# Performance work log

Measured on AMD Instinct MI355X. Metric: run time of the kernel, lower is better.

Reference implementation:

```python
import jax, jax.numpy as jnp
import numpy as np
import math

B, S, HID = 2, 1024, 2048
H, KV, HD = 32, 8, 64
GROUPS = H // KV
KB_N = 4096
THETA = 10000.0


def _rope_cos_sin(position_ids, head_dim, theta=THETA):
    inv_freq = 1.0 / (theta ** (jnp.arange(0, head_dim, 2, dtype=jnp.float32) / head_dim))
    ang = position_ids.astype(jnp.float32)[..., None] * inv_freq  # [B,S,hd/2]
    cos = jnp.concatenate([jnp.cos(ang), jnp.cos(ang)], -1)[:, None]  # [B,1,S,hd]
    sin = jnp.concatenate([jnp.sin(ang), jnp.sin(ang)], -1)[:, None]
    return cos, sin


def _rotate_half(x):
    h = x.shape[-1] // 2
    return jnp.concatenate([-x[..., h:], x[..., :h]], -1)


def _apply_rope(x, cos, sin):
    return x * cos + _rotate_half(x) * sin


def setup_inputs() -> dict:
    key = jax.random.key(0)
    ks = jax.random.split(key, 10)
    hidden_states = jax.random.normal(ks[0], (B, S, HID), dtype=jnp.float32)
    causal = jnp.where(jnp.tril(jnp.ones((S, S), bool)), 0.0, -1e9).astype(jnp.float32)
    attention_mask = jnp.broadcast_to(causal[None, None], (B, 1, S, S)).copy()
    kb_keys = jax.random.normal(ks[1], (B, KB_N, HD), dtype=jnp.float32)
    kb_values = jax.random.normal(ks[2], (B, KB_N, HD), dtype=jnp.float32)
    position_ids = jnp.broadcast_to(jnp.arange(S, dtype=jnp.int64 if jax.config.read('jax_enable_x64') else jnp.int32)[None], (B, S))
    s = 0.02
    Wq = jax.random.normal(ks[3], (HID, HID), dtype=jnp.float32) * s
    Wq_kb = jax.random.normal(ks[4], (HID, HID), dtype=jnp.float32) * s
    Wk = jax.random.normal(ks[5], (KV * HD, HID), dtype=jnp.float32) * s
    Wv = jax.random.normal(ks[6], (KV * HD, HID), dtype=jnp.float32) * s
    Wo = jax.random.normal(ks[7], (HID, HID), dtype=jnp.float32) * s
    score_shift = jnp.zeros((H, 1), dtype=jnp.float32) - 3.0
    return {"hidden_states": hidden_states, "attention_mask": attention_mask,
            "kb_keys": kb_keys, "kb_values": kb_values, "Wq": Wq, "Wq_kb": Wq_kb,
            "Wk": Wk, "Wv": Wv, "Wo": Wo, "score_shift": score_shift,
            "position_ids": position_ids, "top_k": 128}


def reference(hidden_states, attention_mask, kb_keys, kb_values, Wq, Wq_kb, Wk, Wv, Wo, score_shift, position_ids, top_k):
    bsz, q_len, _ = hidden_states.shape
    scale = 1.0 / math.sqrt(HD)
    q = (hidden_states @ Wq.T).reshape(bsz, q_len, H, HD).transpose(0, 2, 1, 3)
    k = (hidden_states @ Wk.T).reshape(bsz, q_len, KV, HD).transpose(0, 2, 1, 3)
    v = (hidden_states @ Wv.T).reshape(bsz, q_len, KV, HD).transpose(0, 2, 1, 3)
    k = jnp.repeat(k, GROUPS, axis=1)  # repeat_kv
    v = jnp.repeat(v, GROUPS, axis=1)
    cos, sin = _rope_cos_sin(position_ids, HD)
    q = _apply_rope(q, cos, sin)
    k = _apply_rope(k, cos, sin)
    attn = jnp.einsum('bhsd,bhtd->bhst', q, k) * scale
    # KB path (layer_idx=0, kb_layer_frequency=1, sep_query_head, dynamic_sparsify)
    qkb = (hidden_states @ Wq_kb.T).reshape(bsz, q_len, H, HD).transpose(0, 2, 1, 3)
    qkb = _apply_rope(qkb, cos, sin)
    kb_scores = jnp.einsum('bhsd,bnd->bhsn', qkb, kb_keys) * scale  # [B,H,S,N]
    # prune_key_value: top-k over head/seq-summed scores, gather keys/values (no grad)
    top_idx = jax.lax.stop_gradient(jax.lax.top_k(kb_scores.sum((1, 2)), top_k)[1])  # [B,k]
    kb_k_g = jax.lax.stop_gradient(jnp.take_along_axis(kb_keys, top_idx[..., None], axis=1))  # [B,k,hd]
    kb_v_g = jax.lax.stop_gradient(jnp.take_along_axis(kb_values, top_idx[..., None], axis=1))
    kb_w = kb_scores[..., :top_k]  # faithful to original: scores of FIRST top_k columns
    kb_w = kb_w + score_shift.reshape(1, H, 1, 1)
    attn_all = jnp.concatenate([attn, kb_w], -1)
    mask_all = jnp.concatenate([attention_mask, jnp.zeros((bsz, 1, q_len, top_k), attention_mask.dtype)], -1)
    attn_all = attn_all + mask_all
    w = jax.nn.softmax(attn_all.astype(jnp.float32), axis=-1).astype(q.dtype)
    out = jnp.einsum('bhst,bhtd->bhsd', w[..., :q_len], v) \
        + jnp.einsum('bhsk,bkd->bhsd', w[..., q_len:], kb_v_g)
    out = out.transpose(0, 2, 1, 3).reshape(bsz, q_len, HID)
    return out @ Wo.T
```

## Files before the change

kernel.cpp:

```cpp
#include <hip/hip_runtime.h>

constexpr int BB   = 2;
constexpr int SEQ  = 1024;
constexpr int HIDC = 2048;
constexpr int NHEAD = 32;
constexpr int NKVH  = 8;
constexpr int HDIM  = 64;
constexpr int KBN   = 4096;
constexpr int TOPK  = 128;
constexpr int HCH   = 16;

typedef unsigned short ushortt;
typedef __attribute__((ext_vector_type(8))) short short8;
typedef __attribute__((ext_vector_type(4))) float f32x4;

__device__ __forceinline__ ushortt f2b(float f){
  union { float f; unsigned u; } v; v.f = f;
  unsigned r = (v.u + 0x7FFFu + ((v.u >> 16) & 1u)) >> 16;
  return (ushortt)r;
}
__device__ __forceinline__ ushortt f2bfast(float f){
  union { float f; unsigned u; } v; v.f = f;
  return (ushortt)((v.u + 0x8000u) >> 16);
}
__device__ __forceinline__ float b2f(ushortt b){
  union { unsigned u; float f; } v; v.u = ((unsigned)b) << 16;
  return v.f;
}
__device__ __forceinline__ void gload16(const void* g, void* l){
  __builtin_amdgcn_global_load_lds((const __attribute__((address_space(1))) void*)g,
                                   (__attribute__((address_space(3))) void*)l, 16, 0, 0);
}

__global__ __launch_bounds__(256) void cast_all(const float* __restrict__ hs,
    const float* __restrict__ Wq, const float* __restrict__ Wqkb,
    const float* __restrict__ Wk, const float* __restrict__ Wv,
    const float* __restrict__ Wo,
    ushortt* __restrict__ hsb, ushortt* __restrict__ Wcatb, ushortt* __restrict__ Wob)
{
  const size_t NHS = (size_t)BB*SEQ*HIDC;
  const size_t NW  = (size_t)5120*HIDC;
  const size_t NO  = (size_t)HIDC*HIDC;
  const size_t total4 = (NHS + NW + NO) / 4;
  for (size_t i = (size_t)blockIdx.x*256 + threadIdx.x; i < total4; i += (size_t)gridDim.x*256){
    size_t e = i * 4;
    const float* src; ushortt* dst;
    if (e < NHS){ src = hs + e; dst = hsb + e; }
    else if (e < NHS + NW){
      size_t ew = e - NHS; dst = Wcatb + ew;
      if      (ew < (size_t)2048*2048) src = Wq   + ew;
      else if (ew < (size_t)4096*2048) src = Wqkb + (ew - (size_t)2048*2048);
      else if (ew < (size_t)4608*2048) src = Wk   + (ew - (size_t)4096*2048);
      else                             src = Wv   + (ew - (size_t)4608*2048);
    } else { size_t eo = e - NHS - NW; src = Wo + eo; dst = Wob + eo; }
    float4 v = *(const float4*)src;
    dst[0] = f2b(v.x); dst[1] = f2b(v.y); dst[2] = f2b(v.z); dst[3] = f2b(v.w);
  }
}

__global__ void rope_table(const int* __restrict__ pos, float* __restrict__ cosT, float* __restrict__ sinT){
  int idx = blockIdx.x*256 + threadIdx.x;
  if (idx >= BB*SEQ*32) return;
  int i = idx & 31; int bs = idx >> 5;
  int p = pos[bs];
  double invf = exp(-(double)i * (log(10000.0) / 32.0));
  double ang = (double)p * invf;
  cosT[idx] = (float)cos(ang);
  sinT[idx] = (float)sin(ang);
}

template<int OUTF32>
__global__ __launch_bounds__(256) void gemm_bt(const ushortt* __restrict__ A,
                                               const ushortt* __restrict__ Bt,
                                               void* __restrict__ Cv,
                                               int M, int N, int K)
{
  __shared__ ushortt As[128*32];
  __shared__ ushortt Bs[128*32];
  const int tid = threadIdx.x;
  const int wave = tid >> 6, lane = tid & 63;
  const int bn = blockIdx.x, bm = blockIdx.y;
  const int wr = (wave >> 1) * 64, wc = (wave & 1) * 64;
  const int l4 = lane >> 4, lm = lane & 15;
  f32x4 acc[4][4] = {};
  const int srow = wave*16 + (lane >> 2);
  const int scol = (lane & 3) * 8;
  const ushortt* Ag0 = A  + (size_t)(bm*128 + srow)*K + scol;
  const ushortt* Ag1 = Ag0 + (size_t)64*K;
  const ushortt* Bg0 = Bt + (size_t)(bn*128 + srow)*K + scol;
  const ushortt* Bg1 = Bg0 + (size_t)64*K;
  ushortt* la0 = &As[(wave*16)*32];
  ushortt* la1 = &As[(64 + wave*16)*32];
  ushortt* lb0 = &Bs[(wave*16)*32];
  ushortt* lb1 = &Bs[(64 + wave*16)*32];
  const int roff = lm*32 + l4*8;
  for (int k0 = 0; k0 < K; k0 += 32){
    gload16(Ag0 + k0, la0);
    gload16(Ag1 + k0, la1);
    gload16(Bg0 + k0, lb0);
    gload16(Bg1 + k0, lb1);
    __syncthreads();
    short8 af[4], bf_[4];
    #pragma unroll
    for (int mi=0;mi<4;++mi) af[mi]  = *(const short8*)&As[(wr + mi*16)*32 + roff];
    #pragma unroll
    for (int ni=0;ni<4;++ni) bf_[ni] = *(const short8*)&Bs[(wc + ni*16)*32 + roff];
    #pragma unroll
    for (int mi=0;mi<4;++mi)
      #pragma unroll
      for (int ni=0;ni<4;++ni)
        acc[mi][ni] = __builtin_amdgcn_mfma_f32_16x16x32_bf16(af[mi], bf_[ni], acc[mi][ni], 0, 0, 0);
    __syncthreads();
  }
  const int cr = l4*4;
  #pragma unroll
  for (int mi=0;mi<4;++mi)
    #pragma unroll
    for (int ni=0;ni<4;++ni)
      #pragma unroll
      for (int r=0;r<4;++r){
        size_t row = (size_t)bm*128 + wr + mi*16 + cr + r;
        size_t col = (size_t)bn*128 + wc + ni*16 + lm;
        float v = acc[mi][ni][r];
        if (OUTF32) ((float*)Cv)[row*(size_t)N + col] = v;
        else        ((ushortt*)Cv)[row*(size_t)N + col] = f2b(v);
      }
}

__global__ __launch_bounds__(256) void rope_pack(const ushortt* __restrict__ C1,
    const float* __restrict__ cosT, const float* __restrict__ sinT,
    ushortt* __restrict__ qr, ushortt* __restrict__ qkbr,
    ushortt* __restrict__ kr, ushortt* __restrict__ vt)
{
  const int row = blockIdx.x;
  const int b = row >> 10, s = row & 1023;
  const ushortt* cr = C1 + (size_t)row * 5120;
  const float* ct = cosT + (size_t)row * 32;
  const float* st = sinT + (size_t)row * 32;
  for (int j = threadIdx.x; j < 2048; j += 256){
    int h = j >> 6, d = j & 63, i = d & 31;
    float c = ct[i], sn = st[i];
    int jp = (d < 32) ? j + 32 : j - 32;
    float x  = b2f(cr[j]);
    float xp = b2f(cr[jp]);
    float o = (d < 32) ? (x*c - xp*sn) : (x*c + xp*sn);
    qr[((size_t)(b*NHEAD + h)*SEQ + s)*HDIM + d] = f2b(o * 0.125f);
    float y  = b2f(cr[2048 + j]);
    float yp = b2f(cr[2048 + jp]);
    float o2 = (d < 32) ? (y*c - yp*sn) : (y*c + yp*sn);
    qkbr[((size_t)(b*NHEAD + h)*SEQ + s)*HDIM + d] = f2b(o2 * 0.125f);
  }
  for (int j = threadIdx.x; j < 512; j += 256){
    int kvh = j >> 6, d = j & 63, i = d & 31;
    float c = ct[i], sn = st[i];
    int jp = (d < 32) ? j + 32 : j - 32;
    float x  = b2f(cr[4096 + j]);
    float xp = b2f(cr[4096 + jp]);
    float o = (d < 32) ? (x*c - xp*sn) : (x*c + xp*sn);
    kr[((size_t)(b*NKVH + kvh)*SEQ + s)*HDIM + d] = f2b(o);
    vt[((size_t)(b*NKVH + kvh)*HDIM + d)*SEQ + s] = cr[4608 + j];
  }
}

__global__ __launch_bounds__(256) void hcs_kernel(const float* __restrict__ hs,
    const float* __restrict__ cosT, const float* __restrict__ sinT,
    float* __restrict__ HcP, float* __restrict__ HsP)
{
  const int b = blockIdx.z, sc = blockIdx.y;
  const int k = blockIdx.x*256 + threadIdx.x;
  const int sbase = sc * (SEQ / HCH);
  __shared__ float cs[64*32];
  __shared__ float sn[64*32];
  for (int t = threadIdx.x; t < 64*32; t += 256){
    cs[t] = cosT[((size_t)b*SEQ + sbase)*32 + t];
    sn[t] = sinT[((size_t)b*SEQ + sbase)*32 + t];
  }
  __syncthreads();
  float ac[32], as_[32];
  #pragma unroll
  for (int i=0;i<32;++i){ ac[i]=0.f; as_[i]=0.f; }
  const float* hp = hs + ((size_t)b*SEQ + sbase)*HIDC + k;
  for (int s = 0; s < 64; ++s){
    float x = hp[(size_t)s*HIDC];
    #pragma unroll
    for (int q=0;q<8;++q){
      float4 c4 = *(const float4*)&cs[s*32 + q*4];
      float4 s4 = *(const float4*)&sn[s*32 + q*4];
      ac[q*4+0]=fmaf(x,c4.x,ac[q*4+0]); as_[q*4+0]=fmaf(x,s4.x,as_[q*4+0]);
      ac[q*4+1]=fmaf(x,c4.y,ac[q*4+1]); as_[q*4+1]=fmaf(x,s4.y,as_[q*4+1]);
      ac[q*4+2]=fmaf(x,c4.z,ac[q*4+2]); as_[q*4+2]=fmaf(x,s4.z,as_[q*4+2]);
      ac[q*4+3]=fmaf(x,c4.w,ac[q*4+3]); as_[q*4+3]=fmaf(x,s4.w,as_[q*4+3]);
    }
  }
  #pragma unroll
  for (int i=0;i<32;++i){
    HcP[(((size_t)sc*BB + b)*32 + i)*HIDC + k] = ac[i];
    HsP[(((size_t)sc*BB + b)*32 + i)*HIDC + k] = as_[i];
  }
}

__global__ __launch_bounds__(256) void hcs_reduce(const float* __restrict__ HcP,
    const float* __restrict__ HsP, float* __restrict__ Hc, float* __restrict__ Hs)
{
  int idx = blockIdx.x*256 + threadIdx.x;
  if (idx >= BB*32*HIDC) return;
  float a = 0.f, c = 0.f;
  #pragma unroll
  for (int sc = 0; sc < HCH; ++sc){
    a += HcP[(size_t)sc*(BB*32*HIDC) + idx];
    c += HsP[(size_t)sc*(BB*32*HIDC) + idx];
  }
  Hc[idx] = a; Hs[idx] = c;
}

__global__ void wsum_kernel(const float* __restrict__ Wqkb, float* __restrict__ Wsum){
  int idx = blockIdx.x*256 + threadIdx.x;
  if (idx >= 64*HIDC) return;
  int d = idx >> 11, k = idx & 2047;
  float acc = 0.f;
  for (int h2 = 0; h2 < NHEAD; ++h2) acc += Wqkb[(size_t)(h2*64 + d)*HIDC + k];
  Wsum[idx] = acc;
}

__global__ __launch_bounds__(256) void qsum_kernel(const float* __restrict__ Hc,
    const float* __restrict__ Hs, const float* __restrict__ Wsum, float* __restrict__ qsum)
{
  const int b = blockIdx.x >> 6, d = blockIdx.x & 63;
  const int i = d & 31;
  const float* hc = Hc + (size_t)(b*32 + i)*HIDC;
  const float* hn = Hs + (size_t)(b*32 + i)*HIDC;
  const float* w1 = Wsum + (size_t)d*HIDC;
  const float* w2 = Wsum + (size_t)((d < 32) ? d + 32 : d - 32)*HIDC;
  double acc = 0.0;
  for (int k = threadIdx.x; k < HIDC; k += 256){
    double t = (double)hc[k] * (double)w1[k];
    double u = (double)hn[k] * (double)w2[k];
    acc += (d < 32) ? (t - u) : (t + u);
  }
  __shared__ double red[256];
  red[threadIdx.x] = acc; __syncthreads();
  for (int s = 128; s > 0; s >>= 1){
    if (threadIdx.x < s) red[threadIdx.x] += red[threadIdx.x + s];
    __syncthreads();
  }
  if (threadIdx.x == 0) qsum[blockIdx.x] = (float)red[0];
}

__global__ void ssum_kernel(const float* __restrict__ qsum, const float* __restrict__ kbK,
                            float* __restrict__ sout){
  int idx = blockIdx.x*256 + threadIdx.x;
  if (idx >= BB*KBN) return;
  int b = idx >> 12;
  const float* q = qsum + b*64;
  const float* kk = kbK + (size_t)idx*64;
  double acc = 0.0;
  for (int d = 0; d < 64; ++d) acc += (double)q[d] * (double)kk[d];
  sout[idx] = (float)(acc * 0.125);
}

__global__ __launch_bounds__(256) void rank_topk(const float* __restrict__ sout,
                                                 int* __restrict__ sel)
{
  const int b = blockIdx.y, chunk = blockIdx.x;
  __shared__ unsigned long long keys[KBN];
  const int tid = threadIdx.x;
  for (int i = tid; i < KBN; i += 256){
    float v = sout[(size_t)b*KBN + i];
    unsigned u = __float_as_uint(v);
    u = (u & 0x80000000u) ? ~u : (u | 0x80000000u);
    keys[i] = ((unsigned long long)u << 32) | (unsigned)(KBN - 1 - i);
  }
  __syncthreads();
  const int myi = chunk*256 + tid;
  const unsigned long long me = keys[myi];
  int rank = 0;
  for (int j = 0; j < KBN; j += 4){
    unsigned long long k0 = keys[j+0];
    unsigned long long k1 = keys[j+1];
    unsigned long long k2 = keys[j+2];
    unsigned long long k3 = keys[j+3];
    rank += (k0 > me) + (k1 > me) + (k2 > me) + (k3 > me);
  }
  if (rank < TOPK) sel[b*TOPK + rank] = myi;
}

__global__ __launch_bounds__(256) void gather_kb(const int* __restrict__ sel,
    const float* __restrict__ kbK, const float* __restrict__ kbV,
    ushortt* __restrict__ kbkb, ushortt* __restrict__ kbvtg)
{
  const int b = blockIdx.x;
  const int tid = threadIdx.x;
  for (int t = tid; t < TOPK*HDIM; t += 256){
    int j = t >> 6, d = t & 63;
    int idx = sel[b*TOPK + j];
    kbkb[(size_t)(b*TOPK + j)*HDIM + d] = f2b(kbK[((size_t)b*KBN + j)*HDIM + d]);
    kbvtg[((size_t)b*HDIM + d)*TOPK + j] = f2b(kbV[((size_t)b*KBN + idx)*HDIM + d]);
  }
}

__global__ __launch_bounds__(256) void attn_kernel(
    const ushortt* __restrict__ qr, const ushortt* __restrict__ qkbr,
    const ushortt* __restrict__ kr, const ushortt* __restrict__ vt,
    const ushortt* __restrict__ kbkb, const ushortt* __restrict__ kbvtg,
    const float* __restrict__ shf, ushortt* __restrict__ attno)
{
  const int i   = blockIdx.x;
  const int xcd = i & 7;
  const int j   = i >> 3;
  const int chunk = xcd + 8*(j >> 5);
  const int pos   = j & 31;
  const int b  = chunk >> 3;
  const int kv = chunk & 7;
  const int qtg = 7 - (pos >> 2);
  const int h  = kv*4 + (pos & 3);
  const int tid = threadIdx.x;
  const int wave = tid >> 6, lane = tid & 63;
  const int l4 = lane >> 4, lm = lane & 15;
  const int qt = qtg*4 + wave;
  const int s0 = qt * 32;

  __shared__ ushortt Ks[2][64*64];
  __shared__ ushortt Vs[2][64*64];
  __shared__ ushortt P[4][32*72];

  ushortt* Pw = P[wave];
  const ushortt* kbase = kr + (size_t)(b*NKVH + kv)*SEQ*HDIM;
  const ushortt* vbase = vt + (size_t)(b*NKVH + kv)*HDIM*SEQ;

  short8 aq[2][2], aqk[2][2];
  {
    const ushortt* qb  = qr   + ((size_t)(b*NHEAD + h)*SEQ + s0)*HDIM;
    const ushortt* qk2 = qkbr + ((size_t)(b*NHEAD + h)*SEQ + s0)*HDIM;
    #pragma unroll
    for (int mi=0;mi<2;++mi)
      #pragma unroll
      for (int kk=0;kk<2;++kk){
        int offa = (mi*16 + lm)*HDIM + kk*32 + l4*8;
        aq[mi][kk]  = *(const short8*)(qb  + offa);
        aqk[mi][kk] = *(const short8*)(qk2 + offa);
      }
  }
  f32x4 O[2][4] = {};
  float lrow[2][4];
  #pragma unroll
  for (int mi=0;mi<2;++mi)
    #pragma unroll
    for (int r=0;r<4;++r) lrow[mi][r] = 0.f;

  auto stageKV = [&](int t, int bsel){
    const int t0 = t*64;
    #pragma unroll
    for (int r2 = 0; r2 < 2; ++r2){
      int slot = r2*256 + wave*64 + lane;
      int row = slot >> 3, cb = slot & 7;
      int lcb = cb ^ (row & 7);
      ushortt* ldsK = &Ks[bsel][(size_t)(r2*256 + wave*64)*8];
      ushortt* ldsV = &Vs[bsel][(size_t)(r2*256 + wave*64)*8];
      gload16(kbase + (size_t)(t0 + row)*HDIM + lcb*8, ldsK);
      gload16(vbase + (size_t)row*SEQ + t0 + lcb*8, ldsV);
    }
  };

  auto update = [&](f32x4 (&lg)[2][4]){
    #pragma unroll
    for (int mi=0;mi<2;++mi)
      #pragma unroll
      for (int r=0;r<4;++r){
        float ps = 0.f;
        #pragma unroll
        for (int ni=0;ni<4;++ni){
          float p = __expf(lg[mi][ni][r]);
          ushortt pb = f2bfast(p);
          ps += b2f(pb);
          Pw[(mi*16 + l4*4 + r)*72 + ni*16 + lm] = pb;
        }
        lrow[mi][r] += ps;
      }
  };

  auto computeTile = [&](int t, int bsel){
    const int t0 = t*64;
    const ushortt* Kb = Ks[bsel];
    const ushortt* Vb = Vs[bsel];
    f32x4 lg[2][4] = {};
    __builtin_amdgcn_s_setprio(1);
    #pragma unroll
    for (int kk=0;kk<2;++kk)
      #pragma unroll
      for (int ni=0;ni<4;++ni){
        int rr = ni*16 + lm;
        int c  = kk*4 + l4;
        short8 bk = *(const short8*)&Kb[rr*64 + ((c ^ (rr&7))*8)];
        lg[0][ni] = __builtin_amdgcn_mfma_f32_16x16x32_bf16(aq[0][kk], bk, lg[0][ni], 0,0,0);
        lg[1][ni] = __builtin_amdgcn_mfma_f32_16x16x32_bf16(aq[1][kk], bk, lg[1][ni], 0,0,0);
      }
    __builtin_amdgcn_s_setprio(0);
    const bool part = (t0 + 63 > s0);
    if (part){
      #pragma unroll
      for (int mi=0;mi<2;++mi)
        #pragma unroll
        for (int ni=0;ni<4;++ni)
          #pragma unroll
          for (int r=0;r<4;++r){
            int row = s0 + mi*16 + l4*4 + r;
            int col = t0 + ni*16 + lm;
            if (col > row) lg[mi][ni][r] = -1e30f;
          }
    }
    update(lg);
    __builtin_amdgcn_s_setprio(1);
    #pragma unroll
    for (int kk=0;kk<2;++kk){
      short8 pa0 = *(const short8*)&Pw[(lm)*72 + kk*32 + l4*8];
      short8 pa1 = *(const short8*)&Pw[(16 + lm)*72 + kk*32 + l4*8];
      #pragma unroll
      for (int di=0;di<4;++di){
        int rr = di*16 + lm;
        int c  = kk*4 + l4;
        short8 bv = *(const short8*)&Vb[rr*64 + ((c ^ (rr&7))*8)];
        O[0][di] = __builtin_amdgcn_mfma_f32_16x16x32_bf16(pa0, bv, O[0][di], 0,0,0);
        O[1][di] = __builtin_amdgcn_mfma_f32_16x16x32_bf16(pa1, bv, O[1][di], 0,0,0);
      }
    }
    __builtin_amdgcn_s_setprio(0);
  };

  const int nkt   = s0/64 + 1;
  const int NTmax = 2*qtg + 2;

  stageKV(0, 0);
  __syncthreads();
  for (int t = 0; t < NTmax; ++t){
    if (t+1 < NTmax) stageKV(t+1, (t+1)&1);
    if (t < nkt) computeTile(t, t&1);
    __syncthreads();
  }

  {
    const float shift = shf[h];
    const ushortt* kbk = kbkb + (size_t)b*TOPK*HDIM;
    const ushortt* kbv = kbvtg + (size_t)b*HDIM*TOPK;
    #pragma unroll
    for (int jt=0;jt<2;++jt){
      const int j0 = jt*64;
      f32x4 lg[2][4] = {};
      __builtin_amdgcn_s_setprio(1);
      #pragma unroll
      for (int kk=0;kk<2;++kk)
        #pragma unroll
        for (int ni=0;ni<4;++ni){
          short8 bk = *(const short8*)(kbk + (size_t)(j0 + ni*16 + lm)*HDIM + kk*32 + l4*8);
          lg[0][ni] = __builtin_amdgcn_mfma_f32_16x16x32_bf16(aqk[0][kk], bk, lg[0][ni], 0,0,0);
          lg[1][ni] = __builtin_amdgcn_mfma_f32_16x16x32_bf16(aqk[1][kk], bk, lg[1][ni], 0,0,0);
        }
      __builtin_amdgcn_s_setprio(0);
      #pragma unroll
      for (int mi=0;mi<2;++mi)
        #pragma unroll
        for (int ni=0;ni<4;++ni)
          #pragma unroll
          for (int r=0;r<4;++r)
            lg[mi][ni][r] += shift;
      update(lg);
      __builtin_amdgcn_s_setprio(1);
      #pragma unroll
      for (int kk=0;kk<2;++kk){
        short8 pa0 = *(const short8*)&Pw[(lm)*72 + kk*32 + l4*8];
        short8 pa1 = *(const short8*)&Pw[(16 + lm)*72 + kk*32 + l4*8];
        #pragma unroll
        for (int di=0;di<4;++di){
          short8 bv = *(const short8*)(kbv + (size_t)(di*16 + lm)*TOPK + j0 + kk*32 + l4*8);
          O[0][di] = __builtin_amdgcn_mfma_f32_16x16x32_bf16(pa0, bv, O[0][di], 0,0,0);
          O[1][di] = __builtin_amdgcn_mfma_f32_16x16x32_bf16(pa1, bv, O[1][di], 0,0,0);
        }
      }
      __builtin_amdgcn_s_setprio(0);
    }
  }
  #pragma unroll
  for (int mi=0;mi<2;++mi)
    #pragma unroll
    for (int r=0;r<4;++r){
      float ls = lrow[mi][r];
      ls += __shfl_xor(ls, 1);
      ls += __shfl_xor(ls, 2);
      ls += __shfl_xor(ls, 4);
      ls += __shfl_xor(ls, 8);
      lrow[mi][r] = 1.0f / ls;
    }
  #pragma unroll
  for (int mi=0;mi<2;++mi)
    #pragma unroll
    for (int di=0;di<4;++di)
      #pragma unroll
      for (int r=0;r<4;++r){
        float o = O[mi][di][r] * lrow[mi][r];
        attno[(size_t)(b*SEQ + s0 + mi*16 + l4*4 + r)*HIDC + h*HDIM + di*16 + lm] = f2b(o);
      }
}

extern "C" void kernel_launch(void* const* d_in, const int* in_sizes, int n_in,
                              void* d_out, int out_size, void* d_ws, size_t ws_size,
                              hipStream_t stream)
{
  (void)in_sizes; (void)n_in; (void)out_size; (void)ws_size;
  const float* hs   = (const float*)d_in[0];
  const float* kbK  = (const float*)d_in[2];
  const float* kbV  = (const float*)d_in[3];
  const float* Wq   = (const float*)d_in[4];
  const float* Wqkb = (const float*)d_in[5];
  const float* Wk   = (const float*)d_in[6];
  const float* Wv   = (const float*)d_in[7];
  const float* Wo   = (const float*)d_in[8];
  const float* shf  = (const float*)d_in[9];
  const int*   pos  = (const int*)d_in[10];

  char* w = (char*)d_ws;
  size_t off = 0;
  auto alloc = [&](size_t bytes)->void*{
    void* p = w + off; off += (bytes + 255) & ~(size_t)255; return p;
  };
  ushortt* hsb   = (ushortt*)alloc((size_t)2048*2048*2);
  ushortt* Wcatb = (ushortt*)alloc((size_t)5120*2048*2);
  ushortt* Wob   = (ushortt*)alloc((size_t)2048*2048*2);
  ushortt* C1    = (ushortt*)alloc((size_t)2048*5120*2);
  float*   cosT  = (float*)alloc((size_t)BB*SEQ*32*4);
  float*   sinT  = (float*)alloc((size_t)BB*SEQ*32*4);
  ushortt* qr    = (ushortt*)alloc((size_t)BB*NHEAD*SEQ*HDIM*2);
  ushortt* qkbr  = (ushortt*)alloc((size_t)BB*NHEAD*SEQ*HDIM*2);
  ushortt* kr    = (ushortt*)alloc((size_t)BB*NKVH*SEQ*HDIM*2);
  ushortt* vt    = (ushortt*)alloc((size_t)BB*NKVH*SEQ*HDIM*2);
  float*   Hc    = (float*)alloc((size_t)BB*32*HIDC*4);
  float*   Hs    = (float*)alloc((size_t)BB*32*HIDC*4);
  float*   Wsum  = (float*)alloc((size_t)64*HIDC*4);
  float*   qsum  = (float*)alloc((size_t)BB*64*4);
  float*   sbuf  = (float*)alloc((size_t)BB*KBN*4);
  int*     sel   = (int*)alloc((size_t)BB*TOPK*4);
  ushortt* kbkb  = (ushortt*)alloc((size_t)BB*TOPK*HDIM*2);
  ushortt* kbvtg = (ushortt*)alloc((size_t)BB*HDIM*TOPK*2);
  ushortt* attno = (ushortt*)alloc((size_t)2048*2048*2);

  float* HcP = (float*)C1;
  float* HsP = HcP + (size_t)HCH*BB*32*HIDC;

  rope_table<<<dim3(256), dim3(256), 0, stream>>>(pos, cosT, sinT);
  hcs_kernel<<<dim3(8, HCH, BB), dim3(256), 0, stream>>>(hs, cosT, sinT, HcP, HsP);
  hcs_reduce<<<dim3(512), dim3(256), 0, stream>>>(HcP, HsP, Hc, Hs);
  wsum_kernel<<<dim3(512), dim3(256), 0, stream>>>(Wqkb, Wsum);
  qsum_kernel<<<dim3(128), dim3(256), 0, stream>>>(Hc, Hs, Wsum, qsum);
  ssum_kernel<<<dim3(32), dim3(256), 0, stream>>>(qsum, kbK, sbuf);
  rank_topk<<<dim3(KBN/256, BB), dim3(256), 0, stream>>>(sbuf, sel);
  gather_kb<<<dim3(BB), dim3(256), 0, stream>>>(sel, kbK, kbV, kbkb, kbvtg);
  cast_all<<<dim3(2048), dim3(256), 0, stream>>>(hs, Wq, Wqkb, Wk, Wv, Wo, hsb, Wcatb, Wob);
  gemm_bt<0><<<dim3(40, 16), dim3(256), 0, stream>>>(hsb, Wcatb, (void*)C1, 2048, 5120, 2048);
  rope_pack<<<dim3(2048), dim3(256), 0, stream>>>(C1, cosT, sinT, qr, qkbr, kr, vt);
  attn_kernel<<<dim3(512), dim3(256), 0, stream>>>(qr, qkbr, kr, vt, kbkb, kbvtg, shf, attno);
  gemm_bt<1><<<dim3(16, 16), dim3(256), 0, stream>>>(attno, Wob, d_out, 2048, 2048, 2048);
}
```

Measured before the change: 322.5 us.

## Double-buffer GEMM LDS, remap blocks per XCD, split K/V packing into transposing kernel

The GEMM now uses two LDS buffers so the global-to-LDS load of the next K slice overlaps with MFMA work on the current one. Block indices are remapped so each XCD handles a contiguous band of rows, which should improve L2 reuse. K/V rope and V transpose move out of rope_pack into a new kv_pack kernel that does vectorized loads and transposes V through shared memory, replacing the strided scalar stores. This costs one more kernel launch and doubles GEMM LDS use, which may lower occupancy.

```diff
diff --git a/kernel.cpp b/kernel.cpp
--- a/kernel.cpp
+++ b/kernel.cpp
@@ -75,11 +75,17 @@
                                                void* __restrict__ Cv,
                                                int M, int N, int K)
 {
-  __shared__ ushortt As[128*32];
-  __shared__ ushortt Bs[128*32];
+  __shared__ ushortt As[2][128*32];
+  __shared__ ushortt Bs[2][128*32];
   const int tid = threadIdx.x;
   const int wave = tid >> 6, lane = tid & 63;
-  const int bn = blockIdx.x, bm = blockIdx.y;
+  const int lid = blockIdx.y * gridDim.x + blockIdx.x;
+  const int xcd = lid & 7;
+  const int idx = lid >> 3;
+  const int rpx = gridDim.y >> 3;
+  const int q   = idx / gridDim.x;
+  const int bm  = xcd * rpx + q;
+  const int bn  = idx - q * gridDim.x;
   const int wr = (wave >> 1) * 64, wc = (wave & 1) * 64;
   const int l4 = lane >> 4, lm = lane & 15;
   f32x4 acc[4][4] = {};
@@ -89,27 +95,36 @@
   const ushortt* Ag1 = Ag0 + (size_t)64*K;
   const ushortt* Bg0 = Bt + (size_t)(bn*128 + srow)*K + scol;
   const ushortt* Bg1 = Bg0 + (size_t)64*K;
-  ushortt* la0 = &As[(wave*16)*32];
-  ushortt* la1 = &As[(64 + wave*16)*32];
-  ushortt* lb0 = &Bs[(wave*16)*32];
-  ushortt* lb1 = &Bs[(64 + wave*16)*32];
   const int roff = lm*32 + l4*8;
-  for (int k0 = 0; k0 < K; k0 += 32){
-    gload16(Ag0 + k0, la0);
-    gload16(Ag1 + k0, la1);
-    gload16(Bg0 + k0, lb0);
-    gload16(Bg1 + k0, lb1);
-    __syncthreads();
+  const int soff = (wave*16)*32;
+
+  auto stage = [&](int k0, ushortt* a, ushortt* b){
+    gload16(Ag0 + k0, a + soff);
+    gload16(Ag1 + k0, a + 64*32 + soff);
+    gload16(Bg0 + k0, b + soff);
+    gload16(Bg1 + k0, b + 64*32 + soff);
+  };
+  auto compute = [&](const ushortt* a, const ushortt* b){
     short8 af[4], bf_[4];
     #pragma unroll
-    for (int mi=0;mi<4;++mi) af[mi]  = *(const short8*)&As[(wr + mi*16)*32 + roff];
-    #pragma unroll
-    for (int ni=0;ni<4;++ni) bf_[ni] = *(const short8*)&Bs[(wc + ni*16)*32 + roff];
+    for (int mi=0;mi<4;++mi) af[mi]  = *(const short8*)&a[(wr + mi*16)*32 + roff];
+    #pragma unroll
+    for (int ni=0;ni<4;++ni) bf_[ni] = *(const short8*)&b[(wc + ni*16)*32 + roff];
     #pragma unroll
     for (int mi=0;mi<4;++mi)
       #pragma unroll
       for (int ni=0;ni<4;++ni)
         acc[mi][ni] = __builtin_amdgcn_mfma_f32_16x16x32_bf16(af[mi], bf_[ni], acc[mi][ni], 0, 0, 0);
+  };
+
+  stage(0, As[0], Bs[0]);
+  __syncthreads();
+  for (int k0 = 0; k0 < K; k0 += 64){
+    stage(k0 + 32, As[1], Bs[1]);
+    compute(As[0], Bs[0]);
+    __syncthreads();
+    if (k0 + 64 < K) stage(k0 + 64, As[0], Bs[0]);
+    compute(As[1], Bs[1]);
     __syncthreads();
   }
   const int cr = l4*4;
@@ -129,8 +144,7 @@
 
 __global__ __launch_bounds__(256) void rope_pack(const ushortt* __restrict__ C1,
     const float* __restrict__ cosT, const float* __restrict__ sinT,
-    ushortt* __restrict__ qr, ushortt* __restrict__ qkbr,
-    ushortt* __restrict__ kr, ushortt* __restrict__ vt)
+    ushortt* __restrict__ qr, ushortt* __restrict__ qkbr)
 {
   const int row = blockIdx.x;
   const int b = row >> 10, s = row & 1023;
@@ -150,15 +164,48 @@
     float o2 = (d < 32) ? (y*c - yp*sn) : (y*c + yp*sn);
     qkbr[((size_t)(b*NHEAD + h)*SEQ + s)*HDIM + d] = f2b(o2 * 0.125f);
   }
-  for (int j = threadIdx.x; j < 512; j += 256){
-    int kvh = j >> 6, d = j & 63, i = d & 31;
-    float c = ct[i], sn = st[i];
-    int jp = (d < 32) ? j + 32 : j - 32;
-    float x  = b2f(cr[4096 + j]);
-    float xp = b2f(cr[4096 + jp]);
-    float o = (d < 32) ? (x*c - xp*sn) : (x*c + xp*sn);
-    kr[((size_t)(b*NKVH + kvh)*SEQ + s)*HDIM + d] = f2b(o);
-    vt[((size_t)(b*NKVH + kvh)*HDIM + d)*SEQ + s] = cr[4608 + j];
+}
+
+__global__ __launch_bounds__(256) void kv_pack(const ushortt* __restrict__ C1,
+    const float* __restrict__ cosT, const float* __restrict__ sinT,
+    ushortt* __restrict__ kr, ushortt* __restrict__ vt)
+{
+  const int bid = blockIdx.x;
+  const int sc  = bid & 15;
+  const int kvh = (bid >> 4) & 7;
+  const int b   = bid >> 7;
+  const int tid = threadIdx.x;
+  __shared__ ushortt vs[64][66];
+  #pragma unroll
+  for (int it = 0; it < 2; ++it){
+    int slot = it*256 + tid;
+    int s = slot >> 3, dblk = slot & 7;
+    const ushortt* base = C1 + (size_t)(b*SEQ + sc*64 + s)*5120 + kvh*64;
+    short8 v = *(const short8*)(base + 4608 + dblk*8);
+    *(short8*)&vs[s][dblk*8] = v;
+    const ushortt* ksrc = base + 4096;
+    const float* ct = cosT + ((size_t)b*SEQ + sc*64 + s)*32;
+    const float* st = sinT + ((size_t)b*SEQ + sc*64 + s)*32;
+    short8 out;
+    #pragma unroll
+    for (int e=0;e<8;++e){
+      int d = dblk*8 + e, i = d & 31;
+      int dp = (d < 32) ? d + 32 : d - 32;
+      float x = b2f(ksrc[d]), xp = b2f(ksrc[dp]);
+      float o = (d < 32) ? (x*ct[i] - xp*st[i]) : (x*ct[i] + xp*st[i]);
+      out[e] = (short)f2b(o);
+    }
+    *(short8*)&kr[((size_t)(b*NKVH + kvh)*SEQ + sc*64 + s)*HDIM + dblk*8] = out;
+  }
+  __syncthreads();
+  #pragma unroll
+  for (int it = 0; it < 2; ++it){
+    int slot = it*256 + tid;
+    int d = slot >> 3, sblk = slot & 7;
+    short8 out;
+    #pragma unroll
+    for (int e=0;e<8;++e) out[e] = (short)vs[sblk*8 + e][d];
+    *(short8*)&vt[((size_t)(b*NKVH + kvh)*HDIM + d)*SEQ + sc*64 + sblk*8] = out;
   }
 }
 
@@ -554,7 +601,8 @@
   gather_kb<<<dim3(BB), dim3(256), 0, stream>>>(sel, kbK, kbV, kbkb, kbvtg);
   cast_all<<<dim3(2048), dim3(256), 0, stream>>>(hs, Wq, Wqkb, Wk, Wv, Wo, hsb, Wcatb, Wob);
   gemm_bt<0><<<dim3(40, 16), dim3(256), 0, stream>>>(hsb, Wcatb, (void*)C1, 2048, 5120, 2048);
-  rope_pack<<<dim3(2048), dim3(256), 0, stream>>>(C1, cosT, sinT, qr, qkbr, kr, vt);
+  rope_pack<<<dim3(2048), dim3(256), 0, stream>>>(C1, cosT, sinT, qr, qkbr);
+  kv_pack<<<dim3(256), dim3(256), 0, stream>>>(C1, cosT, sinT, kr, vt);
   attn_kernel<<<dim3(512), dim3(256), 0, stream>>>(qr, qkbr, kr, vt, kbkb, kbvtg, shf, attno);
   gemm_bt<1><<<dim3(16, 16), dim3(256), 0, stream>>>(attno, Wob, d_out, 2048, 2048, 2048);
 }
```

After: 310.1 us. -3.8%, faster.
